# Performance work log

Measured on AMD Instinct MI355X. Metric: run time of the kernel, lower is better.

The kernel has to match this reference:

```python
import jax, jax.numpy as jnp
import numpy as np

NUM_HEADS = 16
LN_EPS = 1e-5


def _layernorm(x, g, b):
    mu = jnp.mean(x, axis=-1, keepdims=True)
    var = jnp.mean(jnp.square(x - mu), axis=-1, keepdims=True)
    return (x - mu) * jax.lax.rsqrt(var + LN_EPS) * g + b


def setup_inputs() -> dict:
    key = jax.random.key(0)
    ks = jax.random.split(key, 8)
    B, S, D = 4, 2048, 1024
    s = 0.02  # small init so softmax/layernorm stay well-conditioned
    return {
        "x": jax.random.normal(ks[0], (B, S, D), jnp.float32),
        "wq_w": jax.random.normal(ks[1], (D, D), jnp.float32) * s,
        "wq_b": jnp.zeros((D,), jnp.float32),
        "wk_w": jax.random.normal(ks[2], (D, D), jnp.float32) * s,
        "wk_b": jnp.zeros((D,), jnp.float32),
        "wv_w": jax.random.normal(ks[3], (D, D), jnp.float32) * s,
        "wv_b": jnp.zeros((D,), jnp.float32),
        "ln1_g": jnp.ones((D,), jnp.float32),
        "ln1_b": jnp.zeros((D,), jnp.float32),
        "lin1_w": jax.random.normal(ks[4], (D, D), jnp.float32) * s,
        "lin1_b": jnp.zeros((D,), jnp.float32),
        "ln2_g": jnp.ones((D,), jnp.float32),
        "ln2_b": jnp.zeros((D,), jnp.float32),
    }


def reference(x, wq_w, wq_b, wk_w, wk_b, wv_w, wv_b,
              ln1_g, ln1_b, lin1_w, lin1_b, ln2_g, ln2_b):
    B, S, D = x.shape
    H = NUM_HEADS
    dh = D // H

    def proj(w, b):
        # torch Linear: x @ w.T + b ; split heads -> [B,H,S,dh]
        return (x @ w.T + b).reshape(B, S, H, dh).transpose(0, 2, 1, 3)

    q, k, v = proj(wq_w, wq_b), proj(wk_w, wk_b), proj(wv_w, wv_b)

    scores = jnp.einsum("bhqd,bhkd->bhqk", q, k) / jnp.sqrt(jnp.float32(dh))
    causal = jnp.tril(jnp.ones((S, S), jnp.bool_))  # True = attend
    scores = jnp.where(causal[None, None], scores, -jnp.inf)
    probs = jax.nn.softmax(scores, axis=-1)
    attn = jnp.einsum("bhqk,bhkd->bhqd", probs, v)
    attn = attn.transpose(0, 2, 1, 3).reshape(B, S, D)

    h = _layernorm(x + attn, ln1_g, ln1_b)
    h = _layernorm(h + (h @ lin1_w.T + lin1_b), ln2_g, ln2_b)
    return h
```

## Files before the change

### kernel.cpp

```cpp
#include <hip/hip_runtime.h>
#include <math.h>

#define B_  4
#define S_  2048
#define D_  1024
#define H_  16
#define DH_ 64
#define M_  (B_*S_)

typedef unsigned short ushort_t;
typedef __attribute__((ext_vector_type(8))) __bf16 bf16x8;
typedef __attribute__((ext_vector_type(4))) float f32x4;
typedef __attribute__((ext_vector_type(8))) unsigned short us8;
typedef __attribute__((ext_vector_type(4))) unsigned short us4;

__device__ __forceinline__ ushort_t f2bf(float f) {
    unsigned int u = __float_as_uint(f);
    u = (u + 0x7fffu + ((u >> 16) & 1u)) >> 16;
    return (ushort_t)u;
}
__device__ __forceinline__ float bf2f(ushort_t u) {
    return __uint_as_float(((unsigned int)u) << 16);
}

#define GLD16(gp, lp) __builtin_amdgcn_global_load_lds( \
    (const __attribute__((address_space(1))) void*)(gp), \
    (__attribute__((address_space(3))) void*)(lp), 16, 0, 0)

#define WAIT_VM0()   __builtin_amdgcn_s_waitcnt(0x0F70)
#define WAIT_VM4()   __builtin_amdgcn_s_waitcnt(0x0F74)
#define WAIT_VM8()   __builtin_amdgcn_s_waitcnt(0x0F78)
#define MEMFENCE()   asm volatile("" ::: "memory")

__global__ __launch_bounds__(256)
void cvt_all(const float* __restrict__ x,
             const float* __restrict__ w0, const float* __restrict__ w1,
             const float* __restrict__ w2, const float* __restrict__ w3,
             ushort_t* __restrict__ xd, ushort_t* __restrict__ wd)
{
    const int bid = blockIdx.x;
    const float* s;
    ushort_t* d;
    int i;
    if (bid < 4096) {
        s = x; d = xd; i = bid * 2048 + threadIdx.x * 8;
    } else {
        const int k = (bid - 4096) >> 9;
        const int r = (bid - 4096) & 511;
        s = (k == 0) ? w0 : (k == 1) ? w1 : (k == 2) ? w2 : w3;
        d = wd + (size_t)k * (D_ * D_);
        i = r * 2048 + threadIdx.x * 8;
    }
    float4 a = *(const float4*)(s + i);
    float4 b = *(const float4*)(s + i + 4);
    us8 r8;
    r8[0] = f2bf(a.x); r8[1] = f2bf(a.y); r8[2] = f2bf(a.z); r8[3] = f2bf(a.w);
    r8[4] = f2bf(b.x); r8[5] = f2bf(b.y); r8[6] = f2bf(b.z); r8[7] = f2bf(b.w);
    *(us8*)(d + i) = r8;
}

__global__ __launch_bounds__(256)
void gemm_mfma(const ushort_t* __restrict__ A, const ushort_t* __restrict__ Bw,
               const float* __restrict__ bias0, const float* __restrict__ bias1,
               const float* __restrict__ bias2,
               ushort_t* __restrict__ Yb, ushort_t* __restrict__ Qo,
               ushort_t* __restrict__ Ko, ushort_t* __restrict__ Vo,
               int K, int mode)
{
    __shared__ __align__(16) ushort_t As[3][128 * 32];
    __shared__ __align__(16) ushort_t Bs[3][128 * 32];
    const int t = threadIdx.x;
    const int lane = t & 63, wave = t >> 6;
    const int wm = wave >> 1, wn = wave & 1;
    const int m0 = blockIdx.x * 128, n0 = blockIdx.y * 128;
    const int quad = lane >> 4, l15 = lane & 15;

    const int ch0 = wave * 2, ch1 = wave * 2 + 1;
    const int srow = lane >> 2;
    const int scol = (lane & 3) * 8;
    const ushort_t* Ap0 = A  + (size_t)(m0 + ch0 * 16 + srow) * K + scol;
    const ushort_t* Ap1 = A  + (size_t)(m0 + ch1 * 16 + srow) * K + scol;
    const ushort_t* Bp0 = Bw + (size_t)(n0 + ch0 * 16 + srow) * K + scol;
    const ushort_t* Bp1 = Bw + (size_t)(n0 + ch1 * 16 + srow) * K + scol;

    f32x4 acc[4][4] = {};

    GLD16(Ap0, As[0] + ch0 * 512);
    GLD16(Ap1, As[0] + ch1 * 512);
    GLD16(Bp0, Bs[0] + ch0 * 512);
    GLD16(Bp1, Bs[0] + ch1 * 512);
    GLD16(Ap0 + 32, As[1] + ch0 * 512);
    GLD16(Ap1 + 32, As[1] + ch1 * 512);
    GLD16(Bp0 + 32, Bs[1] + ch0 * 512);
    GLD16(Bp1 + 32, Bs[1] + ch1 * 512);

    const int nk = K >> 5;
    for (int ki = 0; ki < nk; ki++) {
        const int buf = ki % 3;
        if (ki + 2 < nk) {
            const int k2 = (ki + 2) << 5;
            const int b2 = (ki + 2) % 3;
            GLD16(Ap0 + k2, As[b2] + ch0 * 512);
            GLD16(Ap1 + k2, As[b2] + ch1 * 512);
            GLD16(Bp0 + k2, Bs[b2] + ch0 * 512);
            GLD16(Bp1 + k2, Bs[b2] + ch1 * 512);
            WAIT_VM8();
        } else if (ki + 1 < nk) {
            WAIT_VM4();
        } else {
            WAIT_VM0();
        }
        MEMFENCE();
        __builtin_amdgcn_s_barrier();
        MEMFENCE();

        bf16x8 af[4], bfr[4];
        #pragma unroll
        for (int i = 0; i < 4; i++)
            af[i] = *(const bf16x8*)(As[buf] + (64 * wm + 16 * i + l15) * 32 + quad * 8);
        #pragma unroll
        for (int j = 0; j < 4; j++)
            bfr[j] = *(const bf16x8*)(Bs[buf] + (64 * wn + 16 * j + l15) * 32 + quad * 8);
        #pragma unroll
        for (int i = 0; i < 4; i++)
            #pragma unroll
            for (int j = 0; j < 4; j++)
                acc[i][j] = __builtin_amdgcn_mfma_f32_16x16x32_bf16(af[i], bfr[j], acc[i][j], 0, 0, 0);

        MEMFENCE();
        __builtin_amdgcn_s_barrier();
        MEMFENCE();
    }

    #pragma unroll
    for (int j = 0; j < 4; j++) {
        const int n = n0 + 64 * wn + 16 * j + l15;
        if (mode == 1) {
            const float bv = bias0[n];
            #pragma unroll
            for (int i = 0; i < 4; i++) {
                const int mrow = m0 + 64 * wm + 16 * i + quad * 4;
                ushort_t* yp = Yb + (size_t)mrow * D_ + n;
                #pragma unroll
                for (int r = 0; r < 4; r++)
                    yp[(size_t)r * D_] = f2bf(acc[i][j][r] + bv);
            }
        } else {
            const int sel = n >> 10, nn = n & 1023;
            const int hh = nn >> 6, dd = nn & 63;
            const float bv = (sel == 0 ? bias0 : (sel == 1 ? bias1 : bias2))[nn];
            const float scl = (sel == 0) ? 0.18033688f : 1.0f;
            #pragma unroll
            for (int i = 0; i < 4; i++) {
                const int mrow = m0 + 64 * wm + 16 * i + quad * 4;
                const int b = mrow >> 11;
                const int ss = mrow & (S_ - 1);
                if (sel == 2) {
                    us4 pk;
                    #pragma unroll
                    for (int r = 0; r < 4; r++)
                        pk[r] = f2bf(acc[i][j][r] + bv);
                    *(us4*)(Vo + (((size_t)b * H_ + hh) * DH_ + dd) * S_ + ss) = pk;
                } else {
                    ushort_t* dst = (sel == 0) ? Qo : Ko;
                    #pragma unroll
                    for (int r = 0; r < 4; r++) {
                        const float v = (acc[i][j][r] + bv) * scl;
                        dst[(((size_t)b * H_ + hh) * S_ + ss + r) * DH_ + dd] = f2bf(v);
                    }
                }
            }
        }
    }
}

__global__ __launch_bounds__(256, 3)
void attn_mfma(const ushort_t* __restrict__ Qb, const ushort_t* __restrict__ Kb,
               const ushort_t* __restrict__ Vt, ushort_t* __restrict__ outb)
{
    __shared__ __align__(16) ushort_t Ks[2][64 * 64];
    __shared__ __align__(16) ushort_t Vs[2][64 * 64];
    __shared__ __align__(16) ushort_t Ps[8][16 * 72];
    const int t = threadIdx.x, lane = t & 63, w = t >> 6;
    const int bh = blockIdx.x;
    const int qt = 15 - (int)blockIdx.y;
    const int quad = lane >> 4, l15 = lane & 15;
    const int rw = 32 * w;

    const int c0 = 2 * w, c1 = 2 * w + 1;
    const int srow = lane >> 3;
    const int scol = 8 * ((lane & 7) ^ srow);
    const ushort_t* KgB = Kb + (size_t)bh * S_ * DH_;
    const ushort_t* VgB = Vt + (size_t)bh * DH_ * S_;
    const ushort_t* Kg0 = KgB + (size_t)(c0 * 8 + srow) * DH_ + scol;
    const ushort_t* Kg1 = KgB + (size_t)(c1 * 8 + srow) * DH_ + scol;
    const ushort_t* Vg0 = VgB + (size_t)(c0 * 8 + srow) * S_ + scol;
    const ushort_t* Vg1 = VgB + (size_t)(c1 * 8 + srow) * S_ + scol;
    ushort_t* pw0 = Ps[w * 2 + 0];
    ushort_t* pw1 = Ps[w * 2 + 1];
    const int b = bh >> 4, hh = bh & (H_ - 1);

    const int q0 = qt * 128;

    const ushort_t* qp = Qb + ((size_t)bh * S_ + q0 + rw + l15) * DH_ + quad * 8;
    const bf16x8 qf00 = *(const bf16x8*)(qp);
    const bf16x8 qf01 = *(const bf16x8*)(qp + 32);
    const bf16x8 qf10 = *(const bf16x8*)(qp + 16 * DH_);
    const bf16x8 qf11 = *(const bf16x8*)(qp + 16 * DH_ + 32);

    f32x4 o0[4] = {}, o1[4] = {};
    float la0 = 0.f, la1 = 0.f;

    WAIT_VM0();
    MEMFENCE();
    GLD16(Kg0, &Ks[0][c0 * 512]);
    GLD16(Kg1, &Ks[0][c1 * 512]);
    GLD16(Vg0, &Vs[0][c0 * 512]);
    GLD16(Vg1, &Vs[0][c1 * 512]);

    const int qg00 = q0 + rw;
    const int qg10 = q0 + rw + 16;
    const int last = 2 * qt + 1;

    for (int kt = 0; kt <= last; kt++) {
        const int buf = kt & 1;
        const int k0 = kt * 64;
        if (kt < last) {
            const size_t ko = (size_t)(k0 + 64) * DH_;
            GLD16(Kg0 + ko, &Ks[buf ^ 1][c0 * 512]);
            GLD16(Kg1 + ko, &Ks[buf ^ 1][c1 * 512]);
            GLD16(Vg0 + k0 + 64, &Vs[buf ^ 1][c0 * 512]);
            GLD16(Vg1 + k0 + 64, &Vs[buf ^ 1][c1 * 512]);
            WAIT_VM4();
        } else {
            WAIT_VM0();
        }
        MEMFENCE();
        __builtin_amdgcn_s_barrier();
        MEMFENCE();

        if (k0 <= qg10 + 15) {
            const bool a0 = (k0 <= qg00 + 15);
            const ushort_t* kb = Ks[buf];
            const ushort_t* vb = Vs[buf];
            const int xr = l15 & 7;

            bf16x8 kf[4][2];
            #pragma unroll
            for (int ct = 0; ct < 4; ct++)
                #pragma unroll
                for (int h = 0; h < 2; h++)
                    kf[ct][h] = *(const bf16x8*)(kb + (ct * 16 + l15) * 64 +
                                                 8 * ((h * 4 + quad) ^ xr));

            const f32x4 cinit = { -16.f, -16.f, -16.f, -16.f };
            f32x4 sc0[4], sc1[4];
            #pragma unroll
            for (int ct = 0; ct < 4; ct++) { sc0[ct] = cinit; sc1[ct] = cinit; }
            __builtin_amdgcn_s_setprio(1);
            #pragma unroll
            for (int ct = 0; ct < 4; ct++) {
                sc1[ct] = __builtin_amdgcn_mfma_f32_16x16x32_bf16(kf[ct][0], qf10, sc1[ct], 0, 0, 0);
                sc1[ct] = __builtin_amdgcn_mfma_f32_16x16x32_bf16(kf[ct][1], qf11, sc1[ct], 0, 0, 0);
            }
            if (a0) {
                #pragma unroll
                for (int ct = 0; ct < 4; ct++) {
                    sc0[ct] = __builtin_amdgcn_mfma_f32_16x16x32_bf16(kf[ct][0], qf00, sc0[ct], 0, 0, 0);
                    sc0[ct] = __builtin_amdgcn_mfma_f32_16x16x32_bf16(kf[ct][1], qf01, sc0[ct], 0, 0, 0);
                }
            }
            __builtin_amdgcn_s_setprio(0);

            bf16x8 vf[4][2];
            #pragma unroll
            for (int mt = 0; mt < 4; mt++)
                #pragma unroll
                for (int h = 0; h < 2; h++)
                    vf[mt][h] = *(const bf16x8*)(vb + (mt * 16 + l15) * 64 +
                                                 8 * ((h * 4 + quad) ^ xr));

            if (k0 + 63 > qg10) {
                const int qq = qg10 + l15;
                #pragma unroll
                for (int ct = 0; ct < 4; ct++) {
                    const int key = k0 + ct * 16 + quad * 4;
                    #pragma unroll
                    for (int r = 0; r < 4; r++)
                        if (key + r > qq) sc1[ct][r] = -1e30f;
                }
            }
            if (a0 && k0 + 63 > qg00) {
                const int qq = qg00 + l15;
                #pragma unroll
                for (int ct = 0; ct < 4; ct++) {
                    const int key = k0 + ct * 16 + quad * 4;
                    #pragma unroll
                    for (int r = 0; r < 4; r++)
                        if (key + r > qq) sc0[ct][r] = -1e30f;
                }
            }

            #pragma unroll
            for (int ct = 0; ct < 4; ct++) {
                us4 pk;
                #pragma unroll
                for (int r = 0; r < 4; r++) {
                    const float p = exp2f(sc1[ct][r]);
                    la1 += p;
                    pk[r] = (ushort_t)(__float_as_uint(p) >> 16);
                }
                *(us4*)(pw1 + l15 * 72 + ct * 16 + quad * 4) = pk;
            }
            if (a0) {
                #pragma unroll
                for (int ct = 0; ct < 4; ct++) {
                    us4 pk;
                    #pragma unroll
                    for (int r = 0; r < 4; r++) {
                        const float p = exp2f(sc0[ct][r]);
                        la0 += p;
                        pk[r] = (ushort_t)(__float_as_uint(p) >> 16);
                    }
                    *(us4*)(pw0 + l15 * 72 + ct * 16 + quad * 4) = pk;
                }
            }

            __builtin_amdgcn_s_setprio(1);
            const bf16x8 pf10 = *(const bf16x8*)(pw1 + l15 * 72 + quad * 8);
            const bf16x8 pf11 = *(const bf16x8*)(pw1 + l15 * 72 + 32 + quad * 8);
            #pragma unroll
            for (int mt = 0; mt < 4; mt++) {
                o1[mt] = __builtin_amdgcn_mfma_f32_16x16x32_bf16(vf[mt][0], pf10, o1[mt], 0, 0, 0);
                o1[mt] = __builtin_amdgcn_mfma_f32_16x16x32_bf16(vf[mt][1], pf11, o1[mt], 0, 0, 0);
            }
            if (a0) {
                const bf16x8 pf00 = *(const bf16x8*)(pw0 + l15 * 72 + quad * 8);
                const bf16x8 pf01 = *(const bf16x8*)(pw0 + l15 * 72 + 32 + quad * 8);
                #pragma unroll
                for (int mt = 0; mt < 4; mt++) {
                    o0[mt] = __builtin_amdgcn_mfma_f32_16x16x32_bf16(vf[mt][0], pf00, o0[mt], 0, 0, 0);
                    o0[mt] = __builtin_amdgcn_mfma_f32_16x16x32_bf16(vf[mt][1], pf01, o0[mt], 0, 0, 0);
                }
            }
            __builtin_amdgcn_s_setprio(0);
        }
        MEMFENCE();
        __builtin_amdgcn_s_barrier();
        MEMFENCE();
    }

    {
        la0 += __shfl_xor(la0, 16);
        la1 += __shfl_xor(la1, 16);
        la0 += __shfl_xor(la0, 32);
        la1 += __shfl_xor(la1, 32);
        const float inv0 = 1.0f / la0, inv1 = 1.0f / la1;
        const int query0 = q0 + rw + l15;
        ushort_t* ob0 = outb + ((size_t)(b * S_ + query0)) * D_ + hh * DH_ + quad * 4;
        ushort_t* ob1 = ob0 + (size_t)16 * D_;
        #pragma unroll
        for (int mt = 0; mt < 4; mt++) {
            us4 r0, r1;
            #pragma unroll
            for (int r = 0; r < 4; r++) {
                r0[r] = f2bf(o0[mt][r] * inv0);
                r1[r] = f2bf(o1[mt][r] * inv1);
            }
            *(us4*)(ob0 + mt * 16) = r0;
            *(us4*)(ob1 + mt * 16) = r1;
        }
    }
}

__global__ __launch_bounds__(256)
void ln_f32bf(const float* __restrict__ X, const ushort_t* __restrict__ R,
              const float* __restrict__ g, const float* __restrict__ bia,
              ushort_t* __restrict__ out_bf)
{
    const int row = blockIdx.x;
    const int t   = threadIdx.x;
    const float4 xv = ((const float4*)(X + (size_t)row * D_))[t];
    const us4 rv = *(const us4*)(R + (size_t)row * D_ + t * 4);
    float s0 = xv.x + bf2f(rv[0]);
    float s1 = xv.y + bf2f(rv[1]);
    float s2 = xv.z + bf2f(rv[2]);
    float s3 = xv.w + bf2f(rv[3]);

    float sum = s0 + s1 + s2 + s3;
    float sq  = s0*s0 + s1*s1 + s2*s2 + s3*s3;
    #pragma unroll
    for (int off = 32; off > 0; off >>= 1) {
        sum += __shfl_down(sum, off);
        sq  += __shfl_down(sq,  off);
    }
    __shared__ float wsum[4], wsq[4], stat[2];
    const int wid = t >> 6, lane = t & 63;
    if (lane == 0) { wsum[wid] = sum; wsq[wid] = sq; }
    __syncthreads();
    if (t == 0) {
        float S = wsum[0] + wsum[1] + wsum[2] + wsum[3];
        float Q = wsq[0]  + wsq[1]  + wsq[2]  + wsq[3];
        float mean = S * (1.0f / D_);
        float var  = Q * (1.0f / D_) - mean * mean;
        stat[0] = mean;
        stat[1] = rsqrtf(var + 1e-5f);
    }
    __syncthreads();
    const float mean = stat[0], inv = stat[1];
    const float4 gv = ((const float4*)g)[t];
    const float4 bv = ((const float4*)bia)[t];
    us4 ob;
    ob[0] = f2bf((s0 - mean) * inv * gv.x + bv.x);
    ob[1] = f2bf((s1 - mean) * inv * gv.y + bv.y);
    ob[2] = f2bf((s2 - mean) * inv * gv.z + bv.z);
    ob[3] = f2bf((s3 - mean) * inv * gv.w + bv.w);
    *(us4*)(out_bf + (size_t)row * D_ + t * 4) = ob;
}

__global__ __launch_bounds__(256)
void ln_bfbf(const ushort_t* __restrict__ Hb, const ushort_t* __restrict__ Yb,
             const float* __restrict__ g, const float* __restrict__ bia,
             float* __restrict__ outf)
{
    const int row = blockIdx.x;
    const int t   = threadIdx.x;
    const us4 hv = *(const us4*)(Hb + (size_t)row * D_ + t * 4);
    const us4 yv = *(const us4*)(Yb + (size_t)row * D_ + t * 4);
    float s0 = bf2f(hv[0]) + bf2f(yv[0]);
    float s1 = bf2f(hv[1]) + bf2f(yv[1]);
    float s2 = bf2f(hv[2]) + bf2f(yv[2]);
    float s3 = bf2f(hv[3]) + bf2f(yv[3]);

    float sum = s0 + s1 + s2 + s3;
    float sq  = s0*s0 + s1*s1 + s2*s2 + s3*s3;
    #pragma unroll
    for (int off = 32; off > 0; off >>= 1) {
        sum += __shfl_down(sum, off);
        sq  += __shfl_down(sq,  off);
    }
    __shared__ float wsum[4], wsq[4], stat[2];
    const int wid = t >> 6, lane = t & 63;
    if (lane == 0) { wsum[wid] = sum; wsq[wid] = sq; }
    __syncthreads();
    if (t == 0) {
        float S = wsum[0] + wsum[1] + wsum[2] + wsum[3];
        float Q = wsq[0]  + wsq[1]  + wsq[2]  + wsq[3];
        float mean = S * (1.0f / D_);
        float var  = Q * (1.0f / D_) - mean * mean;
        stat[0] = mean;
        stat[1] = rsqrtf(var + 1e-5f);
    }
    __syncthreads();
    const float mean = stat[0], inv = stat[1];
    const float4 gv = ((const float4*)g)[t];
    const float4 bv = ((const float4*)bia)[t];
    float4 o;
    o.x = (s0 - mean) * inv * gv.x + bv.x;
    o.y = (s1 - mean) * inv * gv.y + bv.y;
    o.z = (s2 - mean) * inv * gv.z + bv.z;
    o.w = (s3 - mean) * inv * gv.w + bv.w;
    ((float4*)(outf + (size_t)row * D_))[t] = o;
}

extern "C" void kernel_launch(void* const* d_in, const int* in_sizes, int n_in,
                              void* d_out, int out_size, void* d_ws, size_t ws_size,
                              hipStream_t stream)
{
    const float* x      = (const float*)d_in[0];
    const float* wq_w   = (const float*)d_in[1];
    const float* wq_b   = (const float*)d_in[2];
    const float* wk_w   = (const float*)d_in[3];
    const float* wk_b   = (const float*)d_in[4];
    const float* wv_w   = (const float*)d_in[5];
    const float* wv_b   = (const float*)d_in[6];
    const float* ln1_g  = (const float*)d_in[7];
    const float* ln1_b  = (const float*)d_in[8];
    const float* lin1_w = (const float*)d_in[9];
    const float* lin1_b = (const float*)d_in[10];
    const float* ln2_g  = (const float*)d_in[11];
    const float* ln2_b  = (const float*)d_in[12];
    float* out = (float*)d_out;

    char* base = (char*)d_ws;
    ushort_t* x_bf    = (ushort_t*)(base);
    ushort_t* attn_bf = (ushort_t*)(base);
    ushort_t* w_bf    = (ushort_t*)(base + 16777216);
    ushort_t* Qbf     = (ushort_t*)(base + 25165824);
    ushort_t* h_bf    = (ushort_t*)(base + 25165824);
    ushort_t* Kbf     = (ushort_t*)(base + 41943040);
    ushort_t* y_bf    = (ushort_t*)(base + 41943040);
    ushort_t* Vtp     = (ushort_t*)(base + 58720256);

    cvt_all<<<dim3(4096 + 4 * 512), 256, 0, stream>>>(
        x, wq_w, wk_w, wv_w, lin1_w, x_bf, w_bf);

    gemm_mfma<<<dim3(M_ / 128, 3072 / 128), 256, 0, stream>>>(
        x_bf, w_bf, wq_b, wk_b, wv_b, nullptr, Qbf, Kbf, Vtp, D_, 0);

    attn_mfma<<<dim3(64, 16), 256, 0, stream>>>(Qbf, Kbf, Vtp, attn_bf);

    ln_f32bf<<<M_, 256, 0, stream>>>(x, attn_bf, ln1_g, ln1_b, h_bf);

    gemm_mfma<<<dim3(M_ / 128, D_ / 128), 256, 0, stream>>>(
        h_bf, w_bf + 3 * D_ * D_, lin1_b, nullptr, nullptr, y_bf, nullptr, nullptr, nullptr, D_, 1);

    ln_bfbf<<<M_, 256, 0, stream>>>(h_bf, y_bf, ln2_g, ln2_b, out);
}
```

Baseline: 293.1 us.

## Add 256x256-tile 8-wave QKV GEMM with swizzled LDS and interleaved pipeline

Replaces the generic 128x128 GEMM for the fused QKV projection with a dedicated kernel using 256x256 output tiles, 512 threads, BK=64 double-buffered XOR-swizzled LDS, and quarter-step interleaving of global-to-LDS staging with MFMA phases. A swizzled block order groups tiles for L2 reuse. The larger tile raises arithmetic intensity and cuts redundant global reads, but the kernel uses one block per CU, runs only 384 blocks, and has many barriers per K step. The old barrier sequences are folded into a BAR macro.

```diff
diff --git a/kernel.cpp b/kernel.cpp
--- a/kernel.cpp
+++ b/kernel.cpp
@@ -31,6 +31,7 @@
 #define WAIT_VM4()   __builtin_amdgcn_s_waitcnt(0x0F74)
 #define WAIT_VM8()   __builtin_amdgcn_s_waitcnt(0x0F78)
 #define MEMFENCE()   asm volatile("" ::: "memory")
+#define BAR()        do { MEMFENCE(); __builtin_amdgcn_s_barrier(); MEMFENCE(); } while (0)
 
 __global__ __launch_bounds__(256)
 void cvt_all(const float* __restrict__ x,
@@ -59,6 +60,166 @@
     *(us8*)(d + i) = r8;
 }
 
+__global__ __launch_bounds__(512, 1)
+void gemm_qkv256(const ushort_t* __restrict__ A, const ushort_t* __restrict__ Bw,
+                 const float* __restrict__ bias0, const float* __restrict__ bias1,
+                 const float* __restrict__ bias2,
+                 ushort_t* __restrict__ Qo, ushort_t* __restrict__ Ko,
+                 ushort_t* __restrict__ Vo)
+{
+    __shared__ __align__(16) ushort_t As[2][16384];
+    __shared__ __align__(16) ushort_t Bs[2][16384];
+
+    const int tid  = threadIdx.x;
+    const int lane = tid & 63, w = tid >> 6;
+    const int wm = w >> 2, wn = w & 3;
+    const int quad = lane >> 4, l15 = lane & 15;
+    const int xr = l15 & 7;
+
+    const int id = blockIdx.x;
+    const int sw = (id & 7) * 48 + (id >> 3);
+    const int m0 = (sw & 31) * 256;
+    const int n0 = (sw >> 5) * 256;
+
+    const int rA = tid >> 3;
+    const int sl = (tid & 7) ^ (rA & 7);
+    const ushort_t* gA = A  + (size_t)(m0 + rA) * 1024 + sl * 8;
+    const ushort_t* gB = Bw + (size_t)(n0 + rA) * 1024 + sl * 8;
+
+#define STAGE_A(bufc, half, kt) do { \
+    GLD16(gA + (size_t)((half)*128 +  0) * 1024 + (kt) * 64, &As[bufc][(half)*8192 +    0 + w*512]); \
+    GLD16(gA + (size_t)((half)*128 + 64) * 1024 + (kt) * 64, &As[bufc][(half)*8192 + 4096 + w*512]); \
+} while (0)
+#define STAGE_B(bufc, half, kt) do { \
+    GLD16(gB + (size_t)((half)*128 +  0) * 1024 + (kt) * 64, &Bs[bufc][(half)*8192 +    0 + w*512]); \
+    GLD16(gB + (size_t)((half)*128 + 64) * 1024 + (kt) * 64, &Bs[bufc][(half)*8192 + 4096 + w*512]); \
+} while (0)
+
+    const ushort_t* Ard0 = &As[0][wm * 8192 + l15 * 64];
+    const ushort_t* Ard1 = &As[1][wm * 8192 + l15 * 64];
+    const ushort_t* Brd0 = &Bs[0][(wn >> 1) * 8192 + ((wn & 1) * 64 + l15) * 64];
+    const ushort_t* Brd1 = &Bs[1][(wn >> 1) * 8192 + ((wn & 1) * 64 + l15) * 64];
+    const int sk0 = (quad ^ xr) * 8;
+    const int sk1 = ((4 + quad) ^ xr) * 8;
+
+    f32x4 acc[8][4] = {};
+    bf16x8 afr[4][2], bfr[4][2];
+
+#define LDA_LO(BASE) do { _Pragma("unroll") \
+    for (int fi_ = 0; fi_ < 4; fi_++) { \
+        afr[fi_][0] = *(const bf16x8*)((BASE) + fi_ * 1024 + sk0); \
+        afr[fi_][1] = *(const bf16x8*)((BASE) + fi_ * 1024 + sk1); } } while (0)
+#define LDA_HI(BASE) do { _Pragma("unroll") \
+    for (int fi_ = 0; fi_ < 4; fi_++) { \
+        afr[fi_][0] = *(const bf16x8*)((BASE) + (4 + fi_) * 1024 + sk0); \
+        afr[fi_][1] = *(const bf16x8*)((BASE) + (4 + fi_) * 1024 + sk1); } } while (0)
+#define LDB2(BASE, FJ0) do { _Pragma("unroll") \
+    for (int fj_ = 0; fj_ < 2; fj_++) { \
+        bfr[(FJ0) + fj_][0] = *(const bf16x8*)((BASE) + ((FJ0) + fj_) * 1024 + sk0); \
+        bfr[(FJ0) + fj_][1] = *(const bf16x8*)((BASE) + ((FJ0) + fj_) * 1024 + sk1); } } while (0)
+#define MFMA_Q(FI0, FJ0) do { \
+    __builtin_amdgcn_s_setprio(1); \
+    _Pragma("unroll") \
+    for (int fi_ = 0; fi_ < 4; fi_++) { \
+        _Pragma("unroll") \
+        for (int fj_ = 0; fj_ < 2; fj_++) { \
+            acc[(FI0)+fi_][(FJ0)+fj_] = __builtin_amdgcn_mfma_f32_16x16x32_bf16( \
+                afr[fi_][0], bfr[(FJ0)+fj_][0], acc[(FI0)+fi_][(FJ0)+fj_], 0, 0, 0); \
+            acc[(FI0)+fi_][(FJ0)+fj_] = __builtin_amdgcn_mfma_f32_16x16x32_bf16( \
+                afr[fi_][1], bfr[(FJ0)+fj_][1], acc[(FI0)+fi_][(FJ0)+fj_], 0, 0, 0); } } \
+    __builtin_amdgcn_s_setprio(0); \
+} while (0)
+
+    STAGE_A(0, 0, 0); STAGE_A(0, 1, 0);
+    STAGE_B(0, 0, 0); STAGE_B(0, 1, 0);
+    STAGE_B(1, 0, 1); STAGE_B(1, 1, 1);
+    WAIT_VM4();
+    BAR();
+
+    for (int t = 0; t < 8; ++t) {
+        const int ktA = 2 * t;
+        const int ktB = 2 * t + 1;
+        const bool more = (t < 7);
+
+        LDA_LO(Ard0); LDB2(Brd0, 0);
+        STAGE_A(1, 0, ktB);
+        BAR();
+        MFMA_Q(0, 0);
+        BAR();
+        LDB2(Brd0, 2);
+        STAGE_A(1, 1, ktB);
+        BAR();
+        MFMA_Q(0, 2);
+        BAR();
+        LDA_HI(Ard0);
+        if (more) STAGE_B(0, 0, ktA + 2);
+        BAR();
+        MFMA_Q(4, 2);
+        BAR();
+        if (more) STAGE_B(0, 1, ktA + 2);
+        BAR();
+        MFMA_Q(4, 0);
+        if (t == 7) WAIT_VM0(); else WAIT_VM4();
+        BAR();
+
+        LDA_LO(Ard1); LDB2(Brd1, 0);
+        if (more) STAGE_A(0, 0, ktA + 2);
+        BAR();
+        MFMA_Q(0, 0);
+        BAR();
+        LDB2(Brd1, 2);
+        if (more) STAGE_A(0, 1, ktA + 2);
+        BAR();
+        MFMA_Q(0, 2);
+        BAR();
+        LDA_HI(Ard1);
+        if (more) STAGE_B(1, 0, ktB + 2);
+        BAR();
+        MFMA_Q(4, 2);
+        BAR();
+        if (more) STAGE_B(1, 1, ktB + 2);
+        BAR();
+        MFMA_Q(4, 0);
+        WAIT_VM4();
+        BAR();
+    }
+
+    #pragma unroll
+    for (int fj = 0; fj < 4; fj++) {
+        const int n = n0 + wn * 64 + fj * 16 + l15;
+        const int sel = n >> 10, nn = n & 1023;
+        const int hh = nn >> 6, dd = nn & 63;
+        const float bv = (sel == 0 ? bias0 : (sel == 1 ? bias1 : bias2))[nn];
+        const float scl = (sel == 0) ? 0.18033688f : 1.0f;
+        #pragma unroll
+        for (int fi = 0; fi < 8; fi++) {
+            const int mrow = m0 + wm * 128 + fi * 16 + quad * 4;
+            const int b = mrow >> 11;
+            const int ss = mrow & (S_ - 1);
+            if (sel == 2) {
+                us4 pk;
+                #pragma unroll
+                for (int r = 0; r < 4; r++)
+                    pk[r] = f2bf(acc[fi][fj][r] + bv);
+                *(us4*)(Vo + (((size_t)b * H_ + hh) * DH_ + dd) * S_ + ss) = pk;
+            } else {
+                ushort_t* dst = (sel == 0) ? Qo : Ko;
+                #pragma unroll
+                for (int r = 0; r < 4; r++) {
+                    const float v = (acc[fi][fj][r] + bv) * scl;
+                    dst[(((size_t)b * H_ + hh) * S_ + ss + r) * DH_ + dd] = f2bf(v);
+                }
+            }
+        }
+    }
+#undef STAGE_A
+#undef STAGE_B
+#undef LDA_LO
+#undef LDA_HI
+#undef LDB2
+#undef MFMA_Q
+}
+
 __global__ __launch_bounds__(256)
 void gemm_mfma(const ushort_t* __restrict__ A, const ushort_t* __restrict__ Bw,
                const float* __restrict__ bias0, const float* __restrict__ bias1,
@@ -110,9 +271,7 @@
         } else {
             WAIT_VM0();
         }
-        MEMFENCE();
-        __builtin_amdgcn_s_barrier();
-        MEMFENCE();
+        BAR();
 
         bf16x8 af[4], bfr[4];
         #pragma unroll
@@ -127,9 +286,7 @@
             for (int j = 0; j < 4; j++)
                 acc[i][j] = __builtin_amdgcn_mfma_f32_16x16x32_bf16(af[i], bfr[j], acc[i][j], 0, 0, 0);
 
-        MEMFENCE();
-        __builtin_amdgcn_s_barrier();
-        MEMFENCE();
+        BAR();
     }
 
     #pragma unroll
@@ -235,9 +392,7 @@
         } else {
             WAIT_VM0();
         }
-        MEMFENCE();
-        __builtin_amdgcn_s_barrier();
-        MEMFENCE();
+        BAR();
 
         if (k0 <= qg10 + 15) {
             const bool a0 = (k0 <= qg00 + 15);
@@ -345,9 +500,7 @@
             }
             __builtin_amdgcn_s_setprio(0);
         }
-        MEMFENCE();
-        __builtin_amdgcn_s_barrier();
-        MEMFENCE();
+        BAR();
     }
 
     {
@@ -495,8 +648,8 @@
     cvt_all<<<dim3(4096 + 4 * 512), 256, 0, stream>>>(
         x, wq_w, wk_w, wv_w, lin1_w, x_bf, w_bf);
 
-    gemm_mfma<<<dim3(M_ / 128, 3072 / 128), 256, 0, stream>>>(
-        x_bf, w_bf, wq_b, wk_b, wv_b, nullptr, Qbf, Kbf, Vtp, D_, 0);
+    gemm_qkv256<<<dim3(384), dim3(512), 0, stream>>>(
+        x_bf, w_bf, wq_b, wk_b, wv_b, Qbf, Kbf, Vtp);
 
     attn_mfma<<<dim3(64, 16), 256, 0, stream>>>(Qbf, Kbf, Vtp, attn_bf);
 
```

Result: slower. 304.3 us (+3.8%).
